# Kernel tuning notes

Measured on AMD Instinct MI355X. Metric: run time of the kernel, lower is better.

Reference implementation:

```python
import math
import jax, jax.numpy as jnp
import numpy as np

N, E, ELG = 10000, 160000, 320000   # nodes, local edges (= line-graph nodes), line-graph edges
D, H = 256, 8                        # ndim == edim, num_heads
DK = D // H


def setup_inputs() -> dict:
    kit = iter(jax.random.split(jax.random.key(0), 64))
    def rn(shape):
        return jax.random.normal(next(kit), shape, jnp.float32)
    def w(i, o):
        return rn((i, o)) * 0.05
    inp = {
        'x': rn((N, D)),
        'local_lgx': rn((E, D)),
        'global_lgx': rn((E, D)),  # unused for graph_view='local' (faithful to source)
        'local_src': jax.random.randint(next(kit), (E,), 0, N, dtype=jnp.int32),
        'local_dst': (jnp.arange(E, dtype=jnp.int32) % N),  # every node has in-edges -> z > 0
        'lg_src': jax.random.randint(next(kit), (ELG,), 0, E, dtype=jnp.int32),
        'lg_dst': (jnp.arange(ELG, dtype=jnp.int32) % E),
        'src_ids': jax.random.randint(next(kit), (E,), 0, N, dtype=jnp.int32),
        'dst_ids': jax.random.randint(next(kit), (E,), 0, N, dtype=jnp.int32),
    }
    for p in ('n', 'e'):
        inp[p + 'Wq'] = w(D, D); inp[p + 'bq'] = jnp.zeros((D,), jnp.float32)
        inp[p + 'Wk'] = w(D, D)
        inp[p + 'Wv'] = w(D, D)
        inp[p + 'Wo'] = w(D, D); inp[p + 'bo'] = jnp.zeros((D,), jnp.float32)
        inp[p + 'ln1g'] = jnp.ones((D,), jnp.float32); inp[p + 'ln1b'] = jnp.zeros((D,), jnp.float32)
        inp[p + 'W1'] = w(D, 4 * D); inp[p + 'b1'] = jnp.zeros((4 * D,), jnp.float32)
        inp[p + 'W2'] = w(4 * D, D); inp[p + 'b2'] = jnp.zeros((D,), jnp.float32)
        inp[p + 'ln2g'] = jnp.ones((D,), jnp.float32); inp[p + 'ln2b'] = jnp.zeros((D,), jnp.float32)
    return inp


def _ln(x, g, b):
    m = x.mean(-1, keepdims=True)
    v = ((x - m) ** 2).mean(-1, keepdims=True)
    return (x - m) * jax.lax.rsqrt(v + 1e-5) * g + b


def _attn(q, k, v, e, src, dst, n):
    # q,k,v: [n,H,DK]; e: [Eg,H,DK] or None; src,dst: [Eg]
    ks = k[src]
    vs = v[src]
    if e is not None:
        ks = ks + e
        vs = vs + e
    # src_dot_dst + scaled_exp (with clamp, as in lgesql)
    score = jnp.exp(jnp.clip((ks * q[dst]).sum(-1) / math.sqrt(DK), -10.0, 10.0))  # [Eg,H]
    wv = jax.ops.segment_sum(vs * score[..., None], dst, num_segments=n)  # [n,H,DK]
    z = jax.ops.segment_sum(score, dst, num_segments=n)                    # [n,H]
    return wv / z[..., None]


def _block(res, o, Wo, bo, g1, b1, W1, bf1, W2, bf2, g2, b2):
    # layernorm(res + affine_o(o)) followed by FFN with residual+layernorm
    h = _ln(res + o @ Wo + bo, g1, b1)
    return _ln(h + jax.nn.relu(h @ W1 + bf1) @ W2 + bf2, g2, b2)


def reference(x, local_lgx, global_lgx, local_src, local_dst, lg_src, lg_dst, src_ids, dst_ids,
              nWq, nbq, nWk, nWv, nWo, nbo, nln1g, nln1b, nW1, nb1, nW2, nb2, nln2g, nln2b,
              eWq, ebq, eWk, eWv, eWo, ebo, eln1g, eln1b, eW1, eb1, eW2, eb2, eln2g, eln2b):
    # ---- node update (RGATLayer, graph_view='local'); feat_drop=0 (eval) ----
    q = (x @ nWq + nbq).reshape(N, H, DK)
    k = (x @ nWk).reshape(N, H, DK)
    v = (x @ nWv).reshape(N, H, DK)
    e = local_lgx.reshape(E, H, DK)  # edim == ndim -> per-head edge features
    o = _attn(q, k, v, e, local_src, local_dst, N).reshape(N, D)
    out_x = _block(x, o, nWo, nbo, nln1g, nln1b, nW1, nb1, nW2, nb2, nln2g, nln2b)
    # ---- edge update (EdgeRGATLayer on line graph lg) ----
    src_x = x[src_ids]
    dst_x = x[dst_ids]
    qe = (local_lgx @ eWq + ebq + src_x).reshape(E, H, DK)
    ke = (local_lgx @ eWk).reshape(E, H, DK)
    ve = (local_lgx @ eWv + dst_x).reshape(E, H, DK)
    oe = _attn(qe, ke, ve, None, lg_src, lg_dst, E).reshape(E, D)
    out_lgx = _block(local_lgx, oe, eWo, ebo, eln1g, eln1b, eW1, eb1, eW2, eb2, eln2g, eln2b)
    return (out_x, out_lgx)
```

## Files before the change

### kernel.cpp

```cpp
#include <hip/hip_runtime.h>
#include <hip/hip_bf16.h>

typedef __hip_bfloat16 bf16;
typedef __attribute__((ext_vector_type(8))) short short8v;
typedef __attribute__((ext_vector_type(4))) float float4v;

#define N_NODES 10000
#define E_EDGES 160000

__device__ __forceinline__ float b2f(bf16 v){ return __bfloat162float(v); }
__device__ __forceinline__ bf16 f2b(float v){ return __float2bfloat16(v); }

union U8 { int4 v; bf16 h[8]; };
union U4 { int2 v; bf16 h[4]; };

__device__ __forceinline__ float ldx(const void* p, size_t i, bool isb){
    return isb ? b2f(((const bf16*)p)[i]) : ((const float*)p)[i];
}
__device__ __forceinline__ void ld8(const void* p, size_t i, bool isb, float* o){
    if (isb) {
        U8 u; u.v = *reinterpret_cast<const int4*>((const bf16*)p + i);
        #pragma unroll
        for (int j = 0; j < 8; j++) o[j] = b2f(u.h[j]);
    } else {
        const float4* q = reinterpret_cast<const float4*>((const float*)p + i);
        float4 a = q[0], b = q[1];
        o[0]=a.x; o[1]=a.y; o[2]=a.z; o[3]=a.w; o[4]=b.x; o[5]=b.y; o[6]=b.z; o[7]=b.w;
    }
}
__device__ __forceinline__ void stx(void* p, size_t i, bool isb, float v){
    if (isb) ((bf16*)p)[i] = f2b(v); else ((float*)p)[i] = v;
}

typedef const __attribute__((address_space(1))) void* gas_p;
typedef __attribute__((address_space(3))) void* las_p;
__device__ __forceinline__ void gl16(const bf16* g, bf16* l){
    __builtin_amdgcn_global_load_lds((gas_p)g, (las_p)l, 16, 0, 0);
}

__device__ __forceinline__ void quadT(float* a, int t){
    float x0 = (t & 1) ? a[0] : a[1];
    float y0 = __shfl_xor(x0, 1);
    if (t & 1) a[0] = y0; else a[1] = y0;
    float x1 = (t & 1) ? a[2] : a[3];
    float y1 = __shfl_xor(x1, 1);
    if (t & 1) a[2] = y1; else a[3] = y1;
    float x2 = (t & 2) ? a[0] : a[2];
    float y2 = __shfl_xor(x2, 2);
    if (t & 2) a[0] = y2; else a[2] = y2;
    float x3 = (t & 2) ? a[1] : a[3];
    float y3 = __shfl_xor(x3, 2);
    if (t & 2) a[1] = y3; else a[3] = y3;
}

__device__ __forceinline__ int xcd_swz(int wg, int nwg){
    const int q = nwg >> 3, r = nwg & 7;
    const int xcd = wg & 7, ix = wg >> 3;
    return (xcd < r ? xcd * (q + 1) : r * (q + 1) + (xcd - r) * q) + ix;
}

__global__ void detect_dtype(const unsigned short* __restrict__ xw, int* __restrict__ flag){
    const int lane = threadIdx.x;
    int cnt = 0;
    for (int i = lane; i < 8192; i += 64) {
        const unsigned e = (xw[i] >> 7) & 0xFF;
        if (e == 0 || (e >= 100 && e <= 140)) cnt++;
    }
    #pragma unroll
    for (int off = 32; off >= 1; off >>= 1) cnt += __shfl_xor(cnt, off);
    if (lane == 0) *flag = (cnt >= 6554) ? 1 : 0;
}

__global__ __launch_bounds__(256) void cvt_bf16(
    const void* __restrict__ in, bf16* __restrict__ out, long n8, const int* __restrict__ dflag)
{
    const bool isb = (*dflag != 0);
    const long t = (long)blockIdx.x * 256 + threadIdx.x;
    if (t >= n8) return;
    float f[8]; ld8(in, (size_t)t * 8, isb, f);
    U8 u;
    #pragma unroll
    for (int j = 0; j < 8; j++) u.h[j] = f2b(f[j]);
    *reinterpret_cast<int4*>(&out[t * 8]) = u.v;
}

__global__ __launch_bounds__(256) void pack_wT(
    const void* __restrict__ W, bf16* __restrict__ out,
    int K, int Nmat, const int* __restrict__ dflag)
{
    const bool isb = (*dflag != 0);
    const int idx = blockIdx.x * 256 + threadIdx.x;
    if (idx >= K * Nmat) return;
    const int k = idx / Nmat, n = idx - k * Nmat;
    out[(size_t)n * K + k] = f2b(ldx(W, idx, isb));
}

template<int MODE>
__global__ __launch_bounds__(256) void mg(
    const bf16* __restrict__ A, int M, int K, int NC,
    const bf16* __restrict__ Bt0, const bf16* __restrict__ Bt1, const bf16* __restrict__ Bt2,
    const void* __restrict__ bias,
    const bf16* __restrict__ resid,
    const bf16* __restrict__ xg,
    const int* __restrict__ sidx, const int* __restrict__ didx,
    bf16* __restrict__ C, bf16* __restrict__ C2,
    const int* __restrict__ dflag)
{
    const bool isb = (*dflag != 0);
    __shared__ __align__(16) bf16 Al[128 * 64];
    __shared__ __align__(16) bf16 Bl[128 * 64];
    __shared__ float biasl[128];

    const int tid = threadIdx.x;
    const int lane = tid & 63, wave = tid >> 6;
    const int l15 = lane & 15, g = lane >> 4;
    const int t4 = l15 & 3, qd = l15 >> 2;
    const int wr = wave >> 1, wc = wave & 1;

    const int nwgx = gridDim.x;
    int wg = xcd_swz(blockIdx.y * nwgx + blockIdx.x, nwgx * gridDim.y);
    const int rb = (wg / nwgx) * 128, cb = (wg % nwgx) * 128;

    const bf16* Bsel; int cloc;
    if (MODE == 0 || MODE == 7) {
        const int seg = cb >> 8;
        Bsel = (seg == 0) ? Bt0 : ((seg == 1) ? Bt1 : Bt2);
        cloc = cb & 255;
    } else { Bsel = Bt0; cloc = cb; }

    if (tid < 128) {
        float bv = 0.f;
        const int gc = cb + tid;
        if (MODE == 0 || MODE == 7) { if (gc < 256) bv = ldx(bias, gc, isb); }
        else bv = ldx(bias, gc, isb);
        biasl[tid] = bv;
    }

    const int sp = lane & 7, sr8 = lane >> 3;
    int rls[4]; long arows[4];
    #pragma unroll
    for (int j = 0; j < 4; j++) {
        const int rl = wave * 32 + j * 8 + sr8;
        rls[j] = rl;
        const int gm = rb + rl;
        arows[j] = (gm < M) ? gm : (M - 1);
    }

    float4v acc[4][4];
    #pragma unroll
    for (int i = 0; i < 4; i++)
        #pragma unroll
        for (int j = 0; j < 4; j++)
            acc[i][j] = (float4v){0.f, 0.f, 0.f, 0.f};

    for (int k0 = 0; k0 < K; k0 += 64) {
        #pragma unroll
        for (int j = 0; j < 4; j++) {
            const int rl = rls[j];
            const int pp = sp ^ (rl & 7);
            gl16(A + arows[j] * K + k0 + pp * 8,                 Al + rl * 64 + sp * 8);
            gl16(Bsel + (size_t)(cloc + rl) * K + k0 + pp * 8,   Bl + rl * 64 + sp * 8);
        }
        __syncthreads();
        #pragma unroll
        for (int ks = 0; ks < 2; ks++) {
            short8v av[4], bv[4];
            #pragma unroll
            for (int mi = 0; mi < 4; mi++) {
                const int row = wr * 64 + mi * 16 + l15;
                const int cp = (ks * 4 + g) ^ (row & 7);
                av[mi] = *reinterpret_cast<const short8v*>(&Al[row * 64 + cp * 8]);
            }
            #pragma unroll
            for (int ni = 0; ni < 4; ni++) {
                const int row = wc * 64 + ni * 16 + l15;
                const int cp = (ks * 4 + g) ^ (row & 7);
                bv[ni] = *reinterpret_cast<const short8v*>(&Bl[row * 64 + cp * 8]);
            }
            #pragma unroll
            for (int mi = 0; mi < 4; mi++)
                #pragma unroll
                for (int ni = 0; ni < 4; ni++)
                    acc[mi][ni] = __builtin_amdgcn_mfma_f32_16x16x32_bf16(
                        av[mi], bv[ni], acc[mi][ni], 0, 0, 0);
        }
        __syncthreads();
    }

    #pragma unroll
    for (int mi = 0; mi < 4; mi++) {
        const int grow = rb + wr * 64 + mi * 16 + g * 4 + t4;
        const bool ok = (grow < M);
        int s5 = 0, d5 = 0;
        if (MODE == 7 && ok) {
            if (cb < 256) s5 = sidx[grow];
            else if (cb >= 512) d5 = didx[grow];
        }
        #pragma unroll
        for (int ni = 0; ni < 4; ni++) {
            float a[4];
            #pragma unroll
            for (int r = 0; r < 4; r++) a[r] = acc[mi][ni][r];
            quadT(a, t4);
            if (!ok) continue;
            const int ct = wc * 64 + ni * 16 + qd * 4;
            const int gc = cb + ct;
            if (MODE == 0) {
                if (gc < 256) {
                    #pragma unroll
                    for (int u = 0; u < 4; u++) a[u] += biasl[ct + u];
                }
            }
            if (MODE == 3) {
                #pragma unroll
                for (int u = 0; u < 4; u++) a[u] = fmaxf(a[u] + biasl[ct + u], 0.f);
            }
            if (MODE == 7) {
                if (gc < 256) {
                    U4 xx; xx.v = *reinterpret_cast<const int2*>(&xg[(size_t)s5 * 256 + gc]);
                    #pragma unroll
                    for (int u = 0; u < 4; u++) a[u] += biasl[ct + u] + b2f(xx.h[u]);
                } else if (gc >= 512) {
                    U4 xx; xx.v = *reinterpret_cast<const int2*>(&xg[(size_t)d5 * 256 + (gc - 512)]);
                    #pragma unroll
                    for (int u = 0; u < 4; u++) a[u] += b2f(xx.h[u]);
                }
            }
            U4 o;
            #pragma unroll
            for (int u = 0; u < 4; u++) o.h[u] = f2b(a[u]);
            if (MODE == 7) {
                if (gc < 256) *reinterpret_cast<int2*>(&C[(size_t)grow * 256 + gc]) = o.v;
                else          *reinterpret_cast<int2*>(&C2[(size_t)grow * 512 + (gc - 256)]) = o.v;
            } else {
                *reinterpret_cast<int2*>(&C[(size_t)grow * NC + gc]) = o.v;
            }
        }
    }
}

template<int MODE>
__global__ __launch_bounds__(512) void mgln(
    const bf16* __restrict__ A, int M, int K,
    const bf16* __restrict__ Bt,
    const void* __restrict__ bias,
    const bf16* __restrict__ resid,
    const void* __restrict__ lng, const void* __restrict__ lnb,
    bf16* __restrict__ C, void* __restrict__ outv, long obase,
    const int* __restrict__ dflag)
{
    const bool isb = (*dflag != 0);
    __shared__ __align__(16) bf16 Al[128 * 64];
    __shared__ __align__(16) bf16 Bl[256 * 64];
    __shared__ float biasl[256];
    __shared__ float lngl[256];
    __shared__ float lnbl[256];

    const int tid = threadIdx.x;
    const int lane = tid & 63, wave = tid >> 6;
    const int l15 = lane & 15, g = lane >> 4;
    const int t4 = l15 & 3, qd = l15 >> 2;
    const int wr = wave >> 2, wc = wave & 3;

    const int wg = xcd_swz(blockIdx.y, gridDim.y);
    const int rb = wg * 128;

    if (tid < 256) {
        biasl[tid] = ldx(bias, tid, isb);
        lngl[tid]  = ldx(lng,  tid, isb);
        lnbl[tid]  = ldx(lnb,  tid, isb);
    }

    const int sp = lane & 7, sr8 = lane >> 3;
    int rlA[2]; long arA[2];
    #pragma unroll
    for (int j = 0; j < 2; j++) {
        const int rl = wave * 16 + j * 8 + sr8;
        rlA[j] = rl;
        const int gm = rb + rl;
        arA[j] = (gm < M) ? gm : (M - 1);
    }
    int rlB[4];
    #pragma unroll
    for (int j = 0; j < 4; j++) rlB[j] = wave * 32 + j * 8 + sr8;

    float4v acc[4][4];
    #pragma unroll
    for (int i = 0; i < 4; i++)
        #pragma unroll
        for (int j = 0; j < 4; j++)
            acc[i][j] = (float4v){0.f, 0.f, 0.f, 0.f};

    for (int k0 = 0; k0 < K; k0 += 64) {
        #pragma unroll
        for (int j = 0; j < 2; j++) {
            const int pp = sp ^ (rlA[j] & 7);
            gl16(A + arA[j] * K + k0 + pp * 8, Al + rlA[j] * 64 + sp * 8);
        }
        #pragma unroll
        for (int j = 0; j < 4; j++) {
            const int pp = sp ^ (rlB[j] & 7);
            gl16(Bt + (size_t)rlB[j] * K + k0 + pp * 8, Bl + rlB[j] * 64 + sp * 8);
        }
        __syncthreads();
        #pragma unroll
        for (int ks = 0; ks < 2; ks++) {
            short8v av[4], bv[4];
            #pragma unroll
            for (int mi = 0; mi < 4; mi++) {
                const int row = wr * 64 + mi * 16 + l15;
                const int cp = (ks * 4 + g) ^ (row & 7);
                av[mi] = *reinterpret_cast<const short8v*>(&Al[row * 64 + cp * 8]);
            }
            #pragma unroll
            for (int ni = 0; ni < 4; ni++) {
                const int row = wc * 64 + ni * 16 + l15;
                const int cp = (ks * 4 + g) ^ (row & 7);
                bv[ni] = *reinterpret_cast<const short8v*>(&Bl[row * 64 + cp * 8]);
            }
            #pragma unroll
            for (int mi = 0; mi < 4; mi++)
                #pragma unroll
                for (int ni = 0; ni < 4; ni++)
                    acc[mi][ni] = __builtin_amdgcn_mfma_f32_16x16x32_bf16(
                        av[mi], bv[ni], acc[mi][ni], 0, 0, 0);
        }
        __syncthreads();
    }

    float s1[4] = {0.f,0.f,0.f,0.f}, s2[4] = {0.f,0.f,0.f,0.f};
    #pragma unroll
    for (int mi = 0; mi < 4; mi++) {
        const int grow = rb + wr * 64 + mi * 16 + g * 4 + t4;
        const bool ok = (grow < M);
        #pragma unroll
        for (int ni = 0; ni < 4; ni++) {
            float a[4];
            #pragma unroll
            for (int r = 0; r < 4; r++) a[r] = acc[mi][ni][r];
            quadT(a, t4);
            const int ct = wc * 64 + ni * 16 + qd * 4;
            U4 rr; rr.v = make_int2(0, 0);
            if (ok) rr.v = *reinterpret_cast<const int2*>(&resid[(size_t)grow * 256 + ct]);
            #pragma unroll
            for (int u = 0; u < 4; u++) {
                a[u] += biasl[ct + u] + b2f(rr.h[u]);
                s1[mi] += a[u];
                s2[mi] += a[u] * a[u];
                acc[mi][ni][u] = a[u];
            }
        }
    }
    float* Ps1 = (float*)Al;
    float* Ps2 = Ps1 + 2048;
    #pragma unroll
    for (int mi = 0; mi < 4; mi++) {
        const int rowl = wr * 64 + mi * 16 + g * 4 + t4;
        Ps1[(wc * 4 + qd) * 128 + rowl] = s1[mi];
        Ps2[(wc * 4 + qd) * 128 + rowl] = s2[mi];
    }
    __syncthreads();
    float* Mr  = (float*)Bl;
    float* Rsd = Mr + 128;
    if (tid < 128) {
        float a1 = 0.f, a2 = 0.f;
        #pragma unroll
        for (int k = 0; k < 16; k++) { a1 += Ps1[k * 128 + tid]; a2 += Ps2[k * 128 + tid]; }
        const float mn = a1 * (1.f / 256.f);
        const float var = a2 * (1.f / 256.f) - mn * mn;
        Mr[tid] = mn;
        Rsd[tid] = rsqrtf(fmaxf(var, 0.f) + 1e-5f);
    }
    __syncthreads();
    #pragma unroll
    for (int mi = 0; mi < 4; mi++) {
        const int rowl = wr * 64 + mi * 16 + g * 4 + t4;
        const int grow = rb + rowl;
        if (grow >= M) continue;
        const float mn = Mr[rowl], rd = Rsd[rowl];
        #pragma unroll
        for (int ni = 0; ni < 4; ni++) {
            const int ct = wc * 64 + ni * 16 + qd * 4;
            float o[4];
            #pragma unroll
            for (int u = 0; u < 4; u++)
                o[u] = (acc[mi][ni][u] - mn) * rd * lngl[ct + u] + lnbl[ct + u];
            if (MODE == 8) {
                U4 ob;
                #pragma unroll
                for (int u = 0; u < 4; u++) ob.h[u] = f2b(o[u]);
                *reinterpret_cast<int2*>(&C[(size_t)grow * 256 + ct]) = ob.v;
            } else {
                if (isb) {
                    U4 ob;
                    #pragma unroll
                    for (int u = 0; u < 4; u++) ob.h[u] = f2b(o[u]);
                    *reinterpret_cast<int2*>((bf16*)outv + obase + (size_t)grow * 256 + ct) = ob.v;
                } else {
                    float4 f4 = make_float4(o[0], o[1], o[2], o[3]);
                    *reinterpret_cast<float4*>((float*)outv + obase + (size_t)grow * 256 + ct) = f4;
                }
            }
        }
    }
}

__global__ __launch_bounds__(256) void attn_node(
    const bf16* __restrict__ QKV, const int* __restrict__ lsrc,
    const bf16* __restrict__ lgx16, bf16* __restrict__ O)
{
    const int d = blockIdx.x;
    const int tid = threadIdx.x;
    const float q = b2f(QKV[(size_t)d * 768 + tid]);
    float acc = 0.f, z = 0.f;
    for (int j = 0; j < 16; j++) {
        const int i = d + j * N_NODES;
        const int s = lsrc[i];
        const float e = b2f(lgx16[(size_t)i * 256 + tid]);
        float p = (b2f(QKV[(size_t)s * 768 + 256 + tid]) + e) * q;
        #pragma unroll
        for (int off = 16; off >= 1; off >>= 1) p += __shfl_xor(p, off);
        const float sc = expf(fminf(fmaxf(p * 0.17677669529663687f, -10.f), 10.f));
        const float vv = b2f(QKV[(size_t)s * 768 + 512 + tid]) + e;
        acc += vv * sc; z += sc;
    }
    O[(size_t)d * 256 + tid] = f2b(acc / z);
}

__global__ __launch_bounds__(256) void attn_edge_f(
    const bf16* __restrict__ QE, const bf16* __restrict__ KVE,
    const int* __restrict__ lgsrc, bf16* __restrict__ O, int r0, int rows)
{
    const int b = blockIdx.x;
    if (b >= rows) return;
    const int dst = r0 + b;
    const int tid = threadIdx.x;
    const float q = b2f(QE[(size_t)dst * 256 + tid]);
    float acc = 0.f, z = 0.f;
    #pragma unroll
    for (int j = 0; j < 2; j++) {
        const int s = lgsrc[dst + j * E_EDGES];
        const size_t kr = (size_t)s * 512;
        float p = b2f(KVE[kr + tid]) * q;
        #pragma unroll
        for (int off = 16; off >= 1; off >>= 1) p += __shfl_xor(p, off);
        const float sc = expf(fminf(fmaxf(p * 0.17677669529663687f, -10.f), 10.f));
        acc += b2f(KVE[kr + 256 + tid]) * sc; z += sc;
    }
    O[(size_t)b * 256 + tid] = f2b(acc / z);
}

extern "C" void kernel_launch(void* const* d_in, const int* in_sizes, int n_in,
                              void* d_out, int out_size, void* d_ws, size_t ws_size,
                              hipStream_t stream)
{
    const void* x   = d_in[0];
    const void* lgx = d_in[1];
    const int* local_src = (const int*)d_in[3];
    const int* lg_src    = (const int*)d_in[5];
    const int* src_ids   = (const int*)d_in[7];
    const int* dst_ids   = (const int*)d_in[8];

    const void *nWq = d_in[9],  *nbq = d_in[10], *nWk = d_in[11], *nWv = d_in[12],
               *nWo = d_in[13], *nbo = d_in[14], *nln1g = d_in[15], *nln1b = d_in[16],
               *nW1 = d_in[17], *nb1 = d_in[18], *nW2 = d_in[19], *nb2 = d_in[20],
               *nln2g = d_in[21], *nln2b = d_in[22];
    const void *eWq = d_in[23], *ebq = d_in[24], *eWk = d_in[25], *eWv = d_in[26],
               *eWo = d_in[27], *ebo = d_in[28], *eln1g = d_in[29], *eln1b = d_in[30],
               *eW1 = d_in[31], *eb1 = d_in[32], *eW2 = d_in[33], *eb2 = d_in[34],
               *eln2g = d_in[35], *eln2b = d_in[36];

    const dim3 blk(256);
    const dim3 blk2(512);

    int* dflag = (int*)d_ws;
    detect_dtype<<<1, 64, 0, stream>>>((const unsigned short*)x, dflag);

    bf16* pk = (bf16*)((char*)d_ws + 256);
    bf16 *pnWq = pk,            *pnWk = pk + 65536,   *pnWv = pk + 131072,
         *pnWo = pk + 196608,   *pnW1 = pk + 262144,  *pnW2 = pk + 524288,
         *peWq = pk + 786432,   *peWk = pk + 851968,  *peWv = pk + 917504,
         *peWo = pk + 983040,   *peW1 = pk + 1048576, *peW2 = pk + 1310720;
    bf16* x16   = pk + 1572864;
    bf16* lgx16 = x16 + (size_t)N_NODES * 256;

    cvt_bf16<<<1250,  blk, 0, stream>>>(x,   x16,   (long)N_NODES * 32, dflag);
    cvt_bf16<<<20000, blk, 0, stream>>>(lgx, lgx16, (long)E_EDGES * 32, dflag);

    pack_wT<<<256,  blk, 0, stream>>>(nWq, pnWq, 256, 256,  dflag);
    pack_wT<<<256,  blk, 0, stream>>>(nWk, pnWk, 256, 256,  dflag);
    pack_wT<<<256,  blk, 0, stream>>>(nWv, pnWv, 256, 256,  dflag);
    pack_wT<<<256,  blk, 0, stream>>>(nWo, pnWo, 256, 256,  dflag);
    pack_wT<<<1024, blk, 0, stream>>>(nW1, pnW1, 256, 1024, dflag);
    pack_wT<<<1024, blk, 0, stream>>>(nW2, pnW2, 1024, 256, dflag);
    pack_wT<<<256,  blk, 0, stream>>>(eWq, peWq, 256, 256,  dflag);
    pack_wT<<<256,  blk, 0, stream>>>(eWk, peWk, 256, 256,  dflag);
    pack_wT<<<256,  blk, 0, stream>>>(eWv, peWv, 256, 256,  dflag);
    pack_wT<<<256,  blk, 0, stream>>>(eWo, peWo, 256, 256,  dflag);
    pack_wT<<<1024, blk, 0, stream>>>(eW1, peW1, 256, 1024, dflag);
    pack_wT<<<1024, blk, 0, stream>>>(eW2, peW2, 1024, 256, dflag);

    bf16* QKVN = (bf16*)((char*)d_out + (size_t)N_NODES * 256 * 4);
    bf16* ON   = QKVN + (size_t)N_NODES * 768;
    bf16* HN   = ON   + (size_t)N_NODES * 256;
    bf16* FN   = HN   + (size_t)N_NODES * 256;

    const int gx = (N_NODES + 127) / 128;
    mg<0><<<dim3(6, gx), blk, 0, stream>>>(x16, N_NODES, 256, 768,
        pnWq, pnWk, pnWv, nbq, nullptr, nullptr, nullptr, nullptr,
        QKVN, nullptr, dflag);
    attn_node<<<N_NODES, blk, 0, stream>>>(QKVN, local_src, lgx16, ON);
    mgln<8><<<dim3(1, gx), blk2, 0, stream>>>(ON, N_NODES, 256,
        pnWo, nbo, x16, nln1g, nln1b, HN, nullptr, 0, dflag);
    mg<3><<<dim3(8, gx), blk, 0, stream>>>(HN, N_NODES, 256, 1024,
        pnW1, nullptr, nullptr, nb1, nullptr, nullptr, nullptr, nullptr,
        FN, nullptr, dflag);
    mgln<9><<<dim3(1, gx), blk2, 0, stream>>>(FN, N_NODES, 1024,
        pnW2, nb2, HN, nln2g, nln2b, nullptr, d_out, 0, dflag);

    const size_t hdr = 256 + 3145728 + (size_t)5120000 + (size_t)81920000;
    bf16* KVE = (bf16*)((char*)d_ws + hdr);
    bf16* QE  = KVE + (size_t)E_EDGES * 512;
    char* arena = (char*)(QE + (size_t)E_EDGES * 256);

    const size_t used = hdr + (size_t)E_EDGES * 768 * 2;
    long CH = (long)(((ws_size > used ? ws_size - used : 0) / 3072) / 128 * 128);
    if (CH > E_EDGES) CH = E_EDGES;
    if (CH < 128) CH = 128;

    bf16* OE = (bf16*)arena;
    bf16* HE = OE + (size_t)CH * 256;
    bf16* FE = HE + (size_t)CH * 256;

    const int ge = (E_EDGES + 127) / 128;
    mg<7><<<dim3(6, ge), blk, 0, stream>>>(lgx16, E_EDGES, 256, 768,
        peWq, peWk, peWv, ebq, nullptr, x16, src_ids, dst_ids,
        QE, KVE, dflag);

    for (long r0 = 0; r0 < E_EDGES; r0 += CH) {
        const int rows = (int)(((E_EDGES - r0) < CH) ? (E_EDGES - r0) : CH);
        const int gm = (rows + 127) / 128;

        attn_edge_f<<<rows, blk, 0, stream>>>(QE, KVE, lg_src, OE, (int)r0, rows);
        mgln<8><<<dim3(1, gm), blk2, 0, stream>>>(OE, rows, 256,
            peWo, ebo, lgx16 + (size_t)r0 * 256, eln1g, eln1b, HE, nullptr, 0, dflag);
        mg<3><<<dim3(8, gm), blk, 0, stream>>>(HE, rows, 256, 1024,
            peW1, nullptr, nullptr, eb1, nullptr, nullptr, nullptr, nullptr,
            FE, nullptr, dflag);
        mgln<9><<<dim3(1, gm), blk2, 0, stream>>>(FE, rows, 1024,
            peW2, eb2, HE, eln2g, eln2b, nullptr, d_out,
            (long)N_NODES * 256 + r0 * 256, dflag);
    }
}
```

Before: 1.114 ms.

## Use 256x256 double-buffered GEMM tiles for edge-side projections and FFN

Adds a new GEMM kernel, mg2, that uses 256x256 output tiles with 512 threads, double-buffered LDS staging, and fused epilogues for QKV gather-add, ReLU bias and LayerNorm. The edge path's QKV, Wo+LN, W1 and W2+LN GEMMs now use it, with chunk sizes rounded to 256. The larger tiles raise operand reuse and the double buffer overlaps global loads with MFMA work. In exchange they use 128KB of LDS and many accumulator registers, which may limit occupancy. Bias is now read from global memory inside the epilogue instead of from LDS.

```diff
diff --git a/kernel.cpp b/kernel.cpp
--- a/kernel.cpp
+++ b/kernel.cpp
@@ -100,10 +100,7 @@
     const bf16* __restrict__ A, int M, int K, int NC,
     const bf16* __restrict__ Bt0, const bf16* __restrict__ Bt1, const bf16* __restrict__ Bt2,
     const void* __restrict__ bias,
-    const bf16* __restrict__ resid,
-    const bf16* __restrict__ xg,
-    const int* __restrict__ sidx, const int* __restrict__ didx,
-    bf16* __restrict__ C, bf16* __restrict__ C2,
+    bf16* __restrict__ C,
     const int* __restrict__ dflag)
 {
     const bool isb = (*dflag != 0);
@@ -122,7 +119,7 @@
     const int rb = (wg / nwgx) * 128, cb = (wg % nwgx) * 128;
 
     const bf16* Bsel; int cloc;
-    if (MODE == 0 || MODE == 7) {
+    if (MODE == 0) {
         const int seg = cb >> 8;
         Bsel = (seg == 0) ? Bt0 : ((seg == 1) ? Bt1 : Bt2);
         cloc = cb & 255;
@@ -131,7 +128,7 @@
     if (tid < 128) {
         float bv = 0.f;
         const int gc = cb + tid;
-        if (MODE == 0 || MODE == 7) { if (gc < 256) bv = ldx(bias, gc, isb); }
+        if (MODE == 0) { if (gc < 256) bv = ldx(bias, gc, isb); }
         else bv = ldx(bias, gc, isb);
         biasl[tid] = bv;
     }
@@ -191,11 +188,6 @@
     for (int mi = 0; mi < 4; mi++) {
         const int grow = rb + wr * 64 + mi * 16 + g * 4 + t4;
         const bool ok = (grow < M);
-        int s5 = 0, d5 = 0;
-        if (MODE == 7 && ok) {
-            if (cb < 256) s5 = sidx[grow];
-            else if (cb >= 512) d5 = didx[grow];
-        }
         #pragma unroll
         for (int ni = 0; ni < 4; ni++) {
             float a[4];
@@ -215,26 +207,10 @@
                 #pragma unroll
                 for (int u = 0; u < 4; u++) a[u] = fmaxf(a[u] + biasl[ct + u], 0.f);
             }
-            if (MODE == 7) {
-                if (gc < 256) {
-                    U4 xx; xx.v = *reinterpret_cast<const int2*>(&xg[(size_t)s5 * 256 + gc]);
-                    #pragma unroll
-                    for (int u = 0; u < 4; u++) a[u] += biasl[ct + u] + b2f(xx.h[u]);
-                } else if (gc >= 512) {
-                    U4 xx; xx.v = *reinterpret_cast<const int2*>(&xg[(size_t)d5 * 256 + (gc - 512)]);
-                    #pragma unroll
-                    for (int u = 0; u < 4; u++) a[u] += b2f(xx.h[u]);
-                }
-            }
             U4 o;
             #pragma unroll
             for (int u = 0; u < 4; u++) o.h[u] = f2b(a[u]);
-            if (MODE == 7) {
-                if (gc < 256) *reinterpret_cast<int2*>(&C[(size_t)grow * 256 + gc]) = o.v;
-                else          *reinterpret_cast<int2*>(&C2[(size_t)grow * 512 + (gc - 256)]) = o.v;
-            } else {
-                *reinterpret_cast<int2*>(&C[(size_t)grow * NC + gc]) = o.v;
-            }
+            *reinterpret_cast<int2*>(&C[(size_t)grow * NC + gc]) = o.v;
         }
     }
 }
@@ -405,6 +381,241 @@
     }
 }
 
+template<int MODE>
+__global__ __launch_bounds__(512, 2) void mg2(
+    const bf16* __restrict__ A, int M, int K, int NC,
+    const bf16* __restrict__ Bt0, const bf16* __restrict__ Bt1, const bf16* __restrict__ Bt2,
+    const void* __restrict__ bias,
+    const bf16* __restrict__ resid,
+    const bf16* __restrict__ xg,
+    const int* __restrict__ sidx, const int* __restrict__ didx,
+    bf16* __restrict__ C, bf16* __restrict__ C2,
+    const void* __restrict__ lng, const void* __restrict__ lnb,
+    void* __restrict__ outv, long obase,
+    const int* __restrict__ dflag)
+{
+    constexpr bool LNM = (MODE == 8 || MODE == 9);
+    const bool isb = (*dflag != 0);
+    __shared__ __align__(16) bf16 A0l[256 * 64];
+    __shared__ __align__(16) bf16 B0l[256 * 64];
+    __shared__ __align__(16) bf16 A1l[256 * 64];
+    __shared__ __align__(16) bf16 B1l[256 * 64];
+
+    const int tid = threadIdx.x;
+    const int lane = tid & 63, wave = tid >> 6;
+    const int l15 = lane & 15, g = lane >> 4;
+    const int t4 = l15 & 3, qd = l15 >> 2;
+    const int wr = wave >> 2, wc = wave & 3;
+
+    const int nwgx = gridDim.x;
+    int wg = xcd_swz(blockIdx.y * nwgx + blockIdx.x, nwgx * gridDim.y);
+    const int rb = (wg / nwgx) * 256, cb = (wg % nwgx) * 256;
+    const int seg = (MODE == 7) ? (cb >> 8) : 0;
+
+    const bf16* Bsel;
+    int cloc;
+    if (MODE == 7) { Bsel = (seg == 0) ? Bt0 : ((seg == 1) ? Bt1 : Bt2); cloc = 0; }
+    else           { Bsel = Bt0; cloc = cb; }
+
+    const int sp = lane & 7, sr8 = lane >> 3;
+    int rls[4]; long arows[4];
+    #pragma unroll
+    for (int j = 0; j < 4; j++) {
+        const int rl = wave * 32 + j * 8 + sr8;
+        rls[j] = rl;
+        const int gm = rb + rl;
+        arows[j] = (gm < M) ? gm : (M - 1);
+    }
+
+    float4v acc[8][4];
+    #pragma unroll
+    for (int i = 0; i < 8; i++)
+        #pragma unroll
+        for (int j = 0; j < 4; j++)
+            acc[i][j] = (float4v){0.f, 0.f, 0.f, 0.f};
+
+    auto STAGE = [&](bf16* lA, bf16* lB, int k0) {
+        #pragma unroll
+        for (int j = 0; j < 4; j++) {
+            const int rl = rls[j];
+            const int pp = sp ^ (rl & 7);
+            gl16(A + arows[j] * K + k0 + pp * 8,                 lA + rl * 64 + sp * 8);
+            gl16(Bsel + (size_t)(cloc + rl) * K + k0 + pp * 8,   lB + rl * 64 + sp * 8);
+        }
+    };
+    auto COMPUTE = [&](const bf16* lA, const bf16* lB) {
+        #pragma unroll
+        for (int ks = 0; ks < 2; ks++) {
+            short8v av[8], bv[4];
+            #pragma unroll
+            for (int mi = 0; mi < 8; mi++) {
+                const int row = wr * 128 + mi * 16 + l15;
+                const int cp = (ks * 4 + g) ^ (row & 7);
+                av[mi] = *reinterpret_cast<const short8v*>(&lA[row * 64 + cp * 8]);
+            }
+            #pragma unroll
+            for (int ni = 0; ni < 4; ni++) {
+                const int row = wc * 64 + ni * 16 + l15;
+                const int cp = (ks * 4 + g) ^ (row & 7);
+                bv[ni] = *reinterpret_cast<const short8v*>(&lB[row * 64 + cp * 8]);
+            }
+            #pragma unroll
+            for (int mi = 0; mi < 8; mi++)
+                #pragma unroll
+                for (int ni = 0; ni < 4; ni++)
+                    acc[mi][ni] = __builtin_amdgcn_mfma_f32_16x16x32_bf16(
+                        av[mi], bv[ni], acc[mi][ni], 0, 0, 0);
+        }
+    };
+
+    const int nt = K >> 6;
+    STAGE(A0l, B0l, 0);
+    __syncthreads();
+    for (int t = 0; t + 2 < nt; t += 2) {
+        STAGE(A1l, B1l, (t + 1) * 64);
+        COMPUTE(A0l, B0l);
+        __syncthreads();
+        STAGE(A0l, B0l, (t + 2) * 64);
+        COMPUTE(A1l, B1l);
+        __syncthreads();
+    }
+    STAGE(A1l, B1l, (nt - 1) * 64);
+    COMPUTE(A0l, B0l);
+    __syncthreads();
+    COMPUTE(A1l, B1l);
+
+    if constexpr (!LNM) {
+        #pragma unroll
+        for (int mi = 0; mi < 8; mi++) {
+            const int grow = rb + wr * 128 + mi * 16 + g * 4 + t4;
+            const bool ok = (grow < M);
+            int s5 = 0, d5 = 0;
+            if (MODE == 7 && ok) {
+                if (seg == 0) s5 = sidx[grow];
+                else if (seg == 2) d5 = didx[grow];
+            }
+            #pragma unroll
+            for (int ni = 0; ni < 4; ni++) {
+                float a[4];
+                #pragma unroll
+                for (int r = 0; r < 4; r++) a[r] = acc[mi][ni][r];
+                quadT(a, t4);
+                if (!ok) continue;
+                const int ct = wc * 64 + ni * 16 + qd * 4;
+                if (MODE == 3) {
+                    #pragma unroll
+                    for (int u = 0; u < 4; u++)
+                        a[u] = fmaxf(a[u] + ldx(bias, cb + ct + u, isb), 0.f);
+                    U4 o;
+                    #pragma unroll
+                    for (int u = 0; u < 4; u++) o.h[u] = f2b(a[u]);
+                    *reinterpret_cast<int2*>(&C[(size_t)grow * NC + cb + ct]) = o.v;
+                } else {
+                    if (seg == 0) {
+                        U4 xx; xx.v = *reinterpret_cast<const int2*>(&xg[(size_t)s5 * 256 + ct]);
+                        #pragma unroll
+                        for (int u = 0; u < 4; u++)
+                            a[u] += ldx(bias, ct + u, isb) + b2f(xx.h[u]);
+                        U4 o;
+                        #pragma unroll
+                        for (int u = 0; u < 4; u++) o.h[u] = f2b(a[u]);
+                        *reinterpret_cast<int2*>(&C[(size_t)grow * 256 + ct]) = o.v;
+                    } else if (seg == 1) {
+                        U4 o;
+                        #pragma unroll
+                        for (int u = 0; u < 4; u++) o.h[u] = f2b(a[u]);
+                        *reinterpret_cast<int2*>(&C2[(size_t)grow * 512 + ct]) = o.v;
+                    } else {
+                        U4 xx; xx.v = *reinterpret_cast<const int2*>(&xg[(size_t)d5 * 256 + ct]);
+                        #pragma unroll
+                        for (int u = 0; u < 4; u++) a[u] += b2f(xx.h[u]);
+                        U4 o;
+                        #pragma unroll
+                        for (int u = 0; u < 4; u++) o.h[u] = f2b(a[u]);
+                        *reinterpret_cast<int2*>(&C2[(size_t)grow * 512 + 256 + ct]) = o.v;
+                    }
+                }
+            }
+        }
+    } else {
+        float s1[8] = {0,0,0,0,0,0,0,0}, s2[8] = {0,0,0,0,0,0,0,0};
+        #pragma unroll
+        for (int mi = 0; mi < 8; mi++) {
+            const int grow = rb + wr * 128 + mi * 16 + g * 4 + t4;
+            const bool ok = (grow < M);
+            #pragma unroll
+            for (int ni = 0; ni < 4; ni++) {
+                float a[4];
+                #pragma unroll
+                for (int r = 0; r < 4; r++) a[r] = acc[mi][ni][r];
+                quadT(a, t4);
+                const int ct = wc * 64 + ni * 16 + qd * 4;
+                U4 rr; rr.v = make_int2(0, 0);
+                if (ok) rr.v = *reinterpret_cast<const int2*>(&resid[(size_t)grow * 256 + ct]);
+                #pragma unroll
+                for (int u = 0; u < 4; u++) {
+                    a[u] += ldx(bias, ct + u, isb) + b2f(rr.h[u]);
+                    s1[mi] += a[u];
+                    s2[mi] += a[u] * a[u];
+                    acc[mi][ni][u] = a[u];
+                }
+            }
+        }
+        float* Ps1 = (float*)A0l;
+        float* Ps2 = Ps1 + 4096;
+        #pragma unroll
+        for (int mi = 0; mi < 8; mi++) {
+            const int rowl = wr * 128 + mi * 16 + g * 4 + t4;
+            Ps1[(wc * 4 + qd) * 256 + rowl] = s1[mi];
+            Ps2[(wc * 4 + qd) * 256 + rowl] = s2[mi];
+        }
+        __syncthreads();
+        float* Mr  = (float*)B0l;
+        float* Rsd = Mr + 256;
+        if (tid < 256) {
+            float a1 = 0.f, a2 = 0.f;
+            #pragma unroll
+            for (int k = 0; k < 16; k++) { a1 += Ps1[k * 256 + tid]; a2 += Ps2[k * 256 + tid]; }
+            const float mn = a1 * (1.f / 256.f);
+            const float var = a2 * (1.f / 256.f) - mn * mn;
+            Mr[tid] = mn;
+            Rsd[tid] = rsqrtf(fmaxf(var, 0.f) + 1e-5f);
+        }
+        __syncthreads();
+        #pragma unroll
+        for (int mi = 0; mi < 8; mi++) {
+            const int rowl = wr * 128 + mi * 16 + g * 4 + t4;
+            const int grow = rb + rowl;
+            if (grow >= M) continue;
+            const float mn = Mr[rowl], rd = Rsd[rowl];
+            #pragma unroll
+            for (int ni = 0; ni < 4; ni++) {
+                const int ct = wc * 64 + ni * 16 + qd * 4;
+                float o[4];
+                #pragma unroll
+                for (int u = 0; u < 4; u++)
+                    o[u] = (acc[mi][ni][u] - mn) * rd * ldx(lng, ct + u, isb) + ldx(lnb, ct + u, isb);
+                if (MODE == 8) {
+                    U4 ob;
+                    #pragma unroll
+                    for (int u = 0; u < 4; u++) ob.h[u] = f2b(o[u]);
+                    *reinterpret_cast<int2*>(&C[(size_t)grow * 256 + ct]) = ob.v;
+                } else {
+                    if (isb) {
+                        U4 ob;
+                        #pragma unroll
+                        for (int u = 0; u < 4; u++) ob.h[u] = f2b(o[u]);
+                        *reinterpret_cast<int2*>((bf16*)outv + obase + (size_t)grow * 256 + ct) = ob.v;
+                    } else {
+                        float4 f4 = make_float4(o[0], o[1], o[2], o[3]);
+                        *reinterpret_cast<float4*>((float*)outv + obase + (size_t)grow * 256 + ct) = f4;
+                    }
+                }
+            }
+        }
+    }
+}
+
 __global__ __launch_bounds__(256) void attn_node(
     const bf16* __restrict__ QKV, const int* __restrict__ lsrc,
     const bf16* __restrict__ lgx16, bf16* __restrict__ O)
@@ -507,14 +718,12 @@
 
     const int gx = (N_NODES + 127) / 128;
     mg<0><<<dim3(6, gx), blk, 0, stream>>>(x16, N_NODES, 256, 768,
-        pnWq, pnWk, pnWv, nbq, nullptr, nullptr, nullptr, nullptr,
-        QKVN, nullptr, dflag);
+        pnWq, pnWk, pnWv, nbq, QKVN, dflag);
     attn_node<<<N_NODES, blk, 0, stream>>>(QKVN, local_src, lgx16, ON);
     mgln<8><<<dim3(1, gx), blk2, 0, stream>>>(ON, N_NODES, 256,
         pnWo, nbo, x16, nln1g, nln1b, HN, nullptr, 0, dflag);
     mg<3><<<dim3(8, gx), blk, 0, stream>>>(HN, N_NODES, 256, 1024,
-        pnW1, nullptr, nullptr, nb1, nullptr, nullptr, nullptr, nullptr,
-        FN, nullptr, dflag);
+        pnW1, nullptr, nullptr, nb1, FN, dflag);
     mgln<9><<<dim3(1, gx), blk2, 0, stream>>>(FN, N_NODES, 1024,
         pnW2, nb2, HN, nln2g, nln2b, nullptr, d_out, 0, dflag);
 
@@ -524,31 +733,33 @@
     char* arena = (char*)(QE + (size_t)E_EDGES * 256);
 
     const size_t used = hdr + (size_t)E_EDGES * 768 * 2;
-    long CH = (long)(((ws_size > used ? ws_size - used : 0) / 3072) / 128 * 128);
+    long CH = (long)(((ws_size > used ? ws_size - used : 0) / 3072) / 256 * 256);
     if (CH > E_EDGES) CH = E_EDGES;
-    if (CH < 128) CH = 128;
+    if (CH < 256) CH = 256;
 
     bf16* OE = (bf16*)arena;
     bf16* HE = OE + (size_t)CH * 256;
     bf16* FE = HE + (size_t)CH * 256;
 
-    const int ge = (E_EDGES + 127) / 128;
-    mg<7><<<dim3(6, ge), blk, 0, stream>>>(lgx16, E_EDGES, 256, 768,
+    const int geb = E_EDGES / 256;
+    mg2<7><<<dim3(3, geb), blk2, 0, stream>>>(lgx16, E_EDGES, 256, 768,
         peWq, peWk, peWv, ebq, nullptr, x16, src_ids, dst_ids,
-        QE, KVE, dflag);
+        QE, KVE, nullptr, nullptr, nullptr, 0, dflag);
 
     for (long r0 = 0; r0 < E_EDGES; r0 += CH) {
         const int rows = (int)(((E_EDGES - r0) < CH) ? (E_EDGES - r0) : CH);
-        const int gm = (rows + 127) / 128;
+        const int gm = (rows + 255) / 256;
 
         attn_edge_f<<<rows, blk, 0, stream>>>(QE, KVE, lg_src, OE, (int)r0, rows);
-        mgln<8><<<dim3(1, gm), blk2, 0, stream>>>(OE, rows, 256,
-            peWo, ebo, lgx16 + (size_t)r0 * 256, eln1g, eln1b, HE, nullptr, 0, dflag);
-        mg<3><<<dim3(8, gm), blk, 0, stream>>>(HE, rows, 256, 1024,
+        mg2<8><<<dim3(1, gm), blk2, 0, stream>>>(OE, rows, 256, 256,
+            peWo, nullptr, nullptr, ebo, lgx16 + (size_t)r0 * 256, nullptr, nullptr, nullptr,
+            HE, nullptr, eln1g, eln1b, nullptr, 0, dflag);
+        mg2<3><<<dim3(4, gm), blk2, 0, stream>>>(HE, rows, 256, 1024,
             peW1, nullptr, nullptr, eb1, nullptr, nullptr, nullptr, nullptr,
-            FE, nullptr, dflag);
-        mgln<9><<<dim3(1, gm), blk2, 0, stream>>>(FE, rows, 1024,
-            peW2, eb2, HE, eln2g, eln2b, nullptr, d_out,
+            FE, nullptr, nullptr, nullptr, nullptr, 0, dflag);
+        mg2<9><<<dim3(1, gm), blk2, 0, stream>>>(FE, rows, 1024, 256,
+            peW2, nullptr, nullptr, eb2, HE, nullptr, nullptr, nullptr,
+            nullptr, nullptr, eln2g, eln2b, d_out,
             (long)N_NODES * 256 + r0 * 256, dflag);
     }
 }
```

Measured after the change: 1.568 ms. 40.8% more time.
